# Kernel tuning notes

Measured on AMD Instinct MI355X. Metric: run time of the kernel, lower is better.

The kernel has to match this reference:

```python
import jax, jax.numpy as jnp
import numpy as np

B, C, H, W = 4, 256, 64, 64
R, KH, KW = 4, 3, 3
K = KH * KW  # 9 kernel taps


def _conv2d(x, w, b):
    # plain 3x3 conv, stride 1, pad 1, NCHW
    y = jax.lax.conv_general_dilated(x, w, (1, 1), ((1, 1), (1, 1)),
                                     dimension_numbers=('NCHW', 'OIHW', 'NCHW'))
    return y + b[None, :, None, None]


def _bilinear_sample(x, py, px):
    # x: [B,C,H,W]; py,px: [B,K,H,W] float coords; zero padding outside the image.
    B_, C_, H_, W_ = x.shape
    xf = x.reshape(B_, C_, H_ * W_)
    y0 = jnp.floor(py)
    x0 = jnp.floor(px)
    wy = py - y0
    wx = px - x0
    y0i = y0.astype(jnp.int32)
    x0i = x0.astype(jnp.int32)

    def corner(yi, xi, wgt):
        valid = (yi >= 0) & (yi < H_) & (xi >= 0) & (xi < W_)
        idx = (jnp.clip(yi, 0, H_ - 1) * W_ + jnp.clip(xi, 0, W_ - 1)).reshape(B_, -1)
        vals = jax.vmap(lambda xb, ib: jnp.take(xb, ib, axis=1))(xf, idx)  # [B,C,K*H*W]
        vals = vals.reshape(B_, C_, K, H_, W_)
        w_ = (wgt * valid).astype(x.dtype)[:, None]  # [B,1,K,H,W]
        return vals * w_

    out = corner(y0i, x0i, (1 - wy) * (1 - wx))
    out = out + corner(y0i, x0i + 1, (1 - wy) * wx)
    out = out + corner(y0i + 1, x0i, wy * (1 - wx))
    out = out + corner(y0i + 1, x0i + 1, wy * wx)
    return out  # [B,C,K,H,W]


def _deform_conv(x, offset, weight):
    # DCNv1: offset [B, 2K, H, W], interleaved (dy, dx) per kernel tap.
    B_, C_, H_, W_ = x.shape
    off = offset.reshape(B_, K, 2, H_, W_)
    ky, kx = jnp.meshgrid(jnp.arange(KH), jnp.arange(KW), indexing='ij')
    base_y = (ky.reshape(K) - (KH - 1) // 2).astype(x.dtype)
    base_x = (kx.reshape(K) - (KW - 1) // 2).astype(x.dtype)
    py = (jnp.arange(H_, dtype=x.dtype)[None, None, :, None]
          + base_y[None, :, None, None] + off[:, :, 0])
    px = (jnp.arange(W_, dtype=x.dtype)[None, None, None, :]
          + base_x[None, :, None, None] + off[:, :, 1])
    sampled = _bilinear_sample(x, py, px)  # [B,C,K,H,W]
    wr = weight.reshape(weight.shape[0], C_, K)
    return jnp.einsum('bckhw,ock->bohw', sampled, wr)


def setup_inputs() -> dict:
    key = jax.random.key(0)
    k1, k2, k3 = jax.random.split(key, 3)
    x = jax.random.normal(k1, (B, C, H, W), jnp.float32)
    off_w = jax.random.normal(k2, (R, 2 * K, C, KH, KW), jnp.float32) * 0.01
    off_b = jnp.zeros((R, 2 * K), jnp.float32)
    w = jax.random.normal(k3, (R, C, C, KH, KW), jnp.float32) * (1.0 / np.sqrt(C * K))
    return {"x": x, "off_w": off_w, "off_b": off_b, "w": w}


def reference(x, off_w, off_b, w):
    for r in range(R):  # fixed small layer count
        offset = _conv2d(x, off_w[r], off_b[r])
        x = jax.nn.relu(_deform_conv(x, offset, w[r]))
    return x
```

## Files before the change

kernel.cpp:

```cpp
#include <hip/hip_runtime.h>


#define HW 4096

typedef __attribute__((ext_vector_type(8))) __bf16 bf16x8;
typedef __attribute__((ext_vector_type(4))) float f32x4;
typedef __attribute__((ext_vector_type(8))) unsigned short u16x8;

__device__ inline unsigned int f2bf_bits(float f) {
  unsigned int u = __float_as_uint(f);
  return (u + 0x7fffu + ((u >> 16) & 1u)) >> 16;
}

__device__ inline void wg_barrier_lds() {
  asm volatile("s_waitcnt lgkmcnt(0)" ::: "memory");
  __builtin_amdgcn_s_barrier();
  __builtin_amdgcn_sched_barrier(0);
}

__global__ __launch_bounds__(256) void wpack_kernel(
    const float* __restrict__ w, unsigned short* __restrict__ wph) {
  const int f = blockIdx.x * 256 + threadIdx.x;
  const int j  = f & 7;
  const int l  = (f >> 3) & 63;
  const int nt = (f >> 9) & 15;
  const int q  = (f >> 13) % 72;
  const int r  = f / 589824;
  const int n  = nt * 16 + (l & 15);
  const int kk = q * 32 + ((l >> 4) << 3) + j;
  const int c  = kk & 255, k = kk >> 8;
  wph[f] = (unsigned short)f2bf_bits(w[((r * 256 + n) * 256 + c) * 9 + k]);
}

__global__ __launch_bounds__(256) void offwpack_kernel(
    const float* __restrict__ offw, unsigned short* __restrict__ owph) {
  const int f = blockIdx.x * 256 + threadIdx.x;
  const int j  = f & 7;
  const int l  = (f >> 3) & 63;
  const int nt = (f >> 9) & 1;
  const int q  = (f >> 10) % 72;
  const int r  = f / 73728;
  const int n  = nt * 16 + (l & 15);
  const int kk = q * 32 + ((l >> 4) << 3) + j;
  const int c  = kk & 255, k = kk >> 8;
  const float v = (n < 18) ? offw[((r * 18 + n) * 256 + c) * 9 + k] : 0.f;
  owph[f] = (unsigned short)f2bf_bits(v);
}

__global__ __launch_bounds__(256) void xpose_kernel(
    const float* __restrict__ x, unsigned short* __restrict__ xh) {
  const int p0 = blockIdx.x * 64;
  const int c0 = blockIdx.y * 64;
  const int b  = blockIdx.z;
  __shared__ float sT[64][65];
  const int t = threadIdx.x;
  const int pj = t & 63, ci0 = (t >> 6) * 16;
  const float* __restrict__ xb = x + ((size_t)(b * 256 + c0)) * HW + p0;
#pragma unroll
  for (int u = 0; u < 16; ++u)
    sT[ci0 + u][pj] = xb[(size_t)(ci0 + u) * HW + pj];
  __syncthreads();
  const int pr = t >> 2, cs = (t & 3) * 16;
  u16x8 va, vb;
#pragma unroll
  for (int u = 0; u < 8; ++u) va[u] = (unsigned short)f2bf_bits(sT[cs + u][pr]);
#pragma unroll
  for (int u = 0; u < 8; ++u) vb[u] = (unsigned short)f2bf_bits(sT[cs + 8 + u][pr]);
  const size_t o = ((size_t)b * HW + p0 + pr) * 256 + c0 + cs;
  *(u16x8*)(xh + o) = va;
  *(u16x8*)(xh + o + 8) = vb;
}

__global__ __launch_bounds__(1024, 4) void deform_mfma(
    const unsigned short* __restrict__ xh,
    const unsigned short* __restrict__ owh,
    const float* __restrict__ offb,
    const unsigned short* __restrict__ wph,
    unsigned short* __restrict__ yth,
    float* __restrict__ outf) {
  const int gid = blockIdx.x;
  const int b = (gid & 7) >> 1;
  const int h = ((gid >> 3) << 1) | (gid & 1);
  const int t = threadIdx.x, lane = t & 63, wv = t >> 6;
  const int frow = lane & 15, quad = lane >> 4;
  const int sm = t >> 4, cg = t & 15;

  __shared__ __align__(16) unsigned char smem[55808];
  float* s_cw = (float*)smem;
  int*   s_ci = (int*)(smem + 9216);
  unsigned char* sAb = smem + 18432;
  float* s_off = (float*)(smem + 51200);

  {
    const int kv = wv >> 3, ntO = (wv >> 2) & 1, mtO = wv & 3;
    const int mO = mtO * 16 + frow;
    f32x4 aoc = {0.f, 0.f, 0.f, 0.f};
    const u16x8 z8 = {};
    const size_t xb = (size_t)b * HW;
    const u16x8* __restrict__ owp = (const u16x8*)owh;

#define OHLOAD(k, p, A, Bv)                                                 \
  {                                                                         \
    const int ky = (k) / 3 - 1, kx = (k) % 3 - 1;                           \
    const int hy = h + ky;                                                  \
    const int hyc = hy < 0 ? 0 : (hy > 63 ? 63 : hy);                       \
    const int mx = mO + kx;                                                 \
    const bool v = ((unsigned)hy < 64u) && ((unsigned)mx < 64u);            \
    const int cpx = mx < 0 ? 0 : (mx > 63 ? 63 : mx);                       \
    const size_t abase = (xb + (size_t)(hyc * 64 + cpx)) * 256              \
                         + quad * 8 + kv * 128 + (p) * 64;                  \
    _Pragma("unroll") for (int j = 0; j < 2; ++j) {                         \
      A[j] = *(const u16x8*)(xh + abase + j * 32);                          \
      if (!v) A[j] = z8;                                                    \
    }                                                                       \
    _Pragma("unroll") for (int j = 0; j < 2; ++j)                           \
      Bv[j] = owp[(((k) * 8 + kv * 4 + (p) * 2 + j) * 2 + ntO) * 64 + lane];\
  }

#define OHMFMA(A, Bv)                                                       \
  _Pragma("unroll") for (int j = 0; j < 2; ++j)                             \
    aoc = __builtin_amdgcn_mfma_f32_16x16x32_bf16(                          \
        __builtin_bit_cast(bf16x8, A[j]), __builtin_bit_cast(bf16x8, Bv[j]),\
        aoc, 0, 0, 0);

    u16x8 A0[2], Bv0[2], A1[2], Bv1[2];
    OHLOAD(0, 0, A0, Bv0)
    OHLOAD(0, 1, A1, Bv1)
    OHMFMA(A0, Bv0) OHLOAD(1, 0, A0, Bv0)
    OHMFMA(A1, Bv1) OHLOAD(1, 1, A1, Bv1)
    OHMFMA(A0, Bv0) OHLOAD(2, 0, A0, Bv0)
    OHMFMA(A1, Bv1) OHLOAD(2, 1, A1, Bv1)
    OHMFMA(A0, Bv0) OHLOAD(3, 0, A0, Bv0)
    OHMFMA(A1, Bv1) OHLOAD(3, 1, A1, Bv1)
    OHMFMA(A0, Bv0) OHLOAD(4, 0, A0, Bv0)
    OHMFMA(A1, Bv1) OHLOAD(4, 1, A1, Bv1)
    OHMFMA(A0, Bv0) OHLOAD(5, 0, A0, Bv0)
    OHMFMA(A1, Bv1) OHLOAD(5, 1, A1, Bv1)
    OHMFMA(A0, Bv0) OHLOAD(6, 0, A0, Bv0)
    OHMFMA(A1, Bv1) OHLOAD(6, 1, A1, Bv1)
    OHMFMA(A0, Bv0) OHLOAD(7, 0, A0, Bv0)
    OHMFMA(A1, Bv1) OHLOAD(7, 1, A1, Bv1)
    OHMFMA(A0, Bv0) OHLOAD(8, 0, A0, Bv0)
    OHMFMA(A1, Bv1) OHLOAD(8, 1, A1, Bv1)
    OHMFMA(A0, Bv0)
    OHMFMA(A1, Bv1)
#undef OHLOAD
#undef OHMFMA

    f32x4* redp = (f32x4*)(smem + 18432);
    if (kv == 1) redp[(mtO * 2 + ntO) * 64 + lane] = aoc;
    __syncthreads();
    if (kv == 0) {
      const f32x4 o = redp[(mtO * 2 + ntO) * 64 + lane];
      aoc[0] += o[0]; aoc[1] += o[1]; aoc[2] += o[2]; aoc[3] += o[3];
      const int oc = ntO * 16 + frow;
      if (oc < 18) {
        const float bv = offb[oc];
        const int mb = mtO * 16 + quad * 4;
#pragma unroll
        for (int r = 0; r < 4; ++r) s_off[oc * 64 + mb + r] = aoc[r] + bv;
      }
    }
    __syncthreads();
  }

  if (t < 576) {
    const int k = t >> 6, m = t & 63;
    const int ky = k / 3 - 1, kx = k % 3 - 1;
    const float dy = s_off[(2 * k) * 64 + m];
    const float dx = s_off[(2 * k + 1) * 64 + m];
    const float py = (float)(h + ky) + dy;
    const float px = (float)(m + kx) + dx;
    const float y0f = floorf(py), x0f = floorf(px);
    const float wy = py - y0f, wx = px - x0f;
    const int y0 = (int)y0f, x0 = (int)x0f;
#pragma unroll
    for (int j = 0; j < 4; ++j) {
      const int yi = y0 + (j >> 1), xi = x0 + (j & 1);
      const bool v = (yi >= 0) && (yi < 64) && (xi >= 0) && (xi < 64);
      const float wgt = ((j >> 1) ? wy : 1.f - wy) * ((j & 1) ? wx : 1.f - wx);
      s_cw[(k * 4 + j) * 64 + m] = v ? wgt : 0.f;
      const int yc = yi < 0 ? 0 : (yi > 63 ? 63 : yi);
      const int xc = xi < 0 ? 0 : (xi > 63 ? 63 : xi);
      s_ci[(k * 4 + j) * 64 + m] = yc * 64 + xc;
    }
  }
  __syncthreads();

  f32x4 acc[2][4];
#pragma unroll
  for (int mt = 0; mt < 2; ++mt)
#pragma unroll
    for (int nt = 0; nt < 4; ++nt) acc[mt][nt] = (f32x4){0.f, 0.f, 0.f, 0.f};

  const char* __restrict__ xbc = (const char*)(xh + (size_t)b * HW * 256);
  const u16x8* __restrict__ wp = (const u16x8*)wph;
  const int kv  = wv >> 3;
  const int wmh = (wv >> 2) & 1;
  const int wng = wv & 3;
  const int bfo = wng * 4;

  const int gs = ((sm & 3) << 1) | ((sm >> 2) & 1);
  const int wbA = sm * 128 + ((((cg >> 2) ^ gs)) << 4) + (cg & 3) * 4;
  const int wbL = wbA ^ 64;
  const int gr = ((frow & 3) << 1) | ((frow >> 2) & 1);
  const int rb0 = (wmh * 32 + frow) * 128 + ((quad ^ gr) << 4) + kv * 8192;
  const int rb1 = rb0 + 2048;

  unsigned int G0[4], G1[4];
  u16x8 Bc[4], Bn[4];
  float cwrC[4], cwrN[4];
  int cibC[4], cibN[4];
#pragma unroll
  for (int j = 0; j < 4; ++j) {
    cwrC[j] = s_cw[j * 64 + sm];
    cibC[j] = s_ci[j * 64 + sm] * 512;
  }
#pragma unroll
  for (int j = 0; j < 4; ++j)
    G0[j] = *(const unsigned int*)(xbc + cibC[j] + cg * 4);
#pragma unroll
  for (int j = 0; j < 4; ++j)
    G1[j] = *(const unsigned int*)(xbc + cibC[j] + 64 + cg * 4);
#pragma unroll
  for (int i = 0; i < 4; ++i)
    Bc[i] = wp[(kv * 16 + bfo + i) * 64 + lane];

#define COMBINE_STORE(Gx, BB)                                               \
  {                                                                         \
    float s0 = cwrC[0] * __uint_as_float(Gx[0] << 16);                      \
    float s1 = cwrC[0] * __uint_as_float(Gx[0] & 0xffff0000u);              \
    s0 = fmaf(cwrC[1], __uint_as_float(Gx[1] << 16), s0);                   \
    s1 = fmaf(cwrC[1], __uint_as_float(Gx[1] & 0xffff0000u), s1);           \
    s0 = fmaf(cwrC[2], __uint_as_float(Gx[2] << 16), s0);                   \
    s1 = fmaf(cwrC[2], __uint_as_float(Gx[2] & 0xffff0000u), s1);           \
    s0 = fmaf(cwrC[3], __uint_as_float(Gx[3] << 16), s0);                   \
    s1 = fmaf(cwrC[3], __uint_as_float(Gx[3] & 0xffff0000u), s1);           \
    const __bf16 hb0 = (__bf16)s0, hb1 = (__bf16)s1;                        \
    const unsigned int hv =                                                 \
        (unsigned int)__builtin_bit_cast(unsigned short, hb0) |             \
        ((unsigned int)__builtin_bit_cast(unsigned short, hb1) << 16);      \
    const float d0 = s0 - __uint_as_float(hv << 16);                        \
    const float d1 = s1 - __uint_as_float(hv & 0xffff0000u);                \
    const __bf16 lb0 = (__bf16)d0, lb1 = (__bf16)d1;                        \
    const unsigned int lv =                                                 \
        (unsigned int)__builtin_bit_cast(unsigned short, lb0) |             \
        ((unsigned int)__builtin_bit_cast(unsigned short, lb1) << 16);      \
    *(unsigned int*)(sAb + (BB) + wbA) = hv;                                \
    *(unsigned int*)(sAb + (BB) + wbL) = lv;                                \
  }

#define MFMA_BODY(PBv)                                                      \
  {                                                                         \
    bf16x8 ah[2], al[2];                                                    \
    ah[0] = __builtin_bit_cast(bf16x8, *(const u16x8*)(sAb + (PBv) + rb0)); \
    al[0] = __builtin_bit_cast(bf16x8,                                      \
                               *(const u16x8*)(sAb + (PBv) + (rb0 ^ 64)));  \
    ah[1] = __builtin_bit_cast(bf16x8, *(const u16x8*)(sAb + (PBv) + rb1)); \
    al[1] = __builtin_bit_cast(bf16x8,                                      \
                               *(const u16x8*)(sAb + (PBv) + (rb1 ^ 64)));  \
    __builtin_amdgcn_s_setprio(1);                                          \
    _Pragma("unroll") for (int nt = 0; nt < 4; ++nt) {                      \
      const bf16x8 bv = __builtin_bit_cast(bf16x8, Bc[nt]);                 \
      _Pragma("unroll") for (int mt = 0; mt < 2; ++mt) {                    \
        acc[mt][nt] = __builtin_amdgcn_mfma_f32_16x16x32_bf16(              \
            ah[mt], bv, acc[mt][nt], 0, 0, 0);                              \
        acc[mt][nt] = __builtin_amdgcn_mfma_f32_16x16x32_bf16(              \
            al[mt], bv, acc[mt][nt], 0, 0, 0);                              \
      }                                                                     \
    }                                                                       \
    __builtin_amdgcn_s_setprio(0);                                          \
  }

  for (int k9 = 0; k9 < 9; ++k9) {
#pragma unroll
    for (int sp = 0; sp < 4; ++sp) {
      const int PB = (sp & 1) * 16384;
      COMBINE_STORE(G0, PB)
      COMBINE_STORE(G1, PB + 8192)
      wg_barrier_lds();
      const bool more = (k9 < 8) || (sp < 3);
      if (more) {
        if (sp == 3) {
#pragma unroll
          for (int j = 0; j < 4; ++j) {
            cwrN[j] = s_cw[((k9 + 1) * 4 + j) * 64 + sm];
            cibN[j] = s_ci[((k9 + 1) * 4 + j) * 64 + sm] * 512;
          }
#pragma unroll
          for (int j = 0; j < 4; ++j)
            G0[j] = *(const unsigned int*)(xbc + cibN[j] + cg * 4);
#pragma unroll
          for (int j = 0; j < 4; ++j)
            G1[j] = *(const unsigned int*)(xbc + cibN[j] + 64 + cg * 4);
        } else {
          const int c0b = ((2 * sp + 2) & 7) * 64 + cg * 4;
#pragma unroll
          for (int j = 0; j < 4; ++j)
            G0[j] = *(const unsigned int*)(xbc + cibC[j] + c0b);
#pragma unroll
          for (int j = 0; j < 4; ++j)
            G1[j] = *(const unsigned int*)(xbc + cibC[j] + c0b + 64);
        }
      }
      MFMA_BODY(PB)
      if (more) {
        const int cn = k9 * 8 + 2 * sp + kv + 2;
#pragma unroll
        for (int i = 0; i < 4; ++i)
          Bn[i] = wp[(cn * 16 + bfo + i) * 64 + lane];
#pragma unroll
        for (int i = 0; i < 4; ++i) Bc[i] = Bn[i];
      }
      if (sp == 3 && k9 < 8) {
#pragma unroll
        for (int j = 0; j < 4; ++j) { cwrC[j] = cwrN[j]; cibC[j] = cibN[j]; }
      }
    }
  }
#undef COMBINE_STORE
#undef MFMA_BODY

  __syncthreads();
  {
    float* redb = (float*)sAb;
    const int rbase = ((wv & 7) * 64 + lane) * 16;
#pragma unroll
    for (int ph = 0; ph < 2; ++ph) {
      if (kv == 1) {
#pragma unroll
        for (int mt = 0; mt < 2; ++mt)
#pragma unroll
          for (int q2 = 0; q2 < 2; ++q2)
            *(f32x4*)&redb[rbase + (mt * 2 + q2) * 4] = acc[mt][ph * 2 + q2];
      }
      __syncthreads();
      if (kv == 0) {
#pragma unroll
        for (int mt = 0; mt < 2; ++mt)
#pragma unroll
          for (int q2 = 0; q2 < 2; ++q2) {
            const f32x4 o = *(const f32x4*)&redb[rbase + (mt * 2 + q2) * 4];
            acc[mt][ph * 2 + q2][0] += o[0];
            acc[mt][ph * 2 + q2][1] += o[1];
            acc[mt][ph * 2 + q2][2] += o[2];
            acc[mt][ph * 2 + q2][3] += o[3];
          }
      }
      __syncthreads();
    }
  }

  if (outf) {
    if (kv == 0) {
#pragma unroll
      for (int mt = 0; mt < 2; ++mt)
#pragma unroll
        for (int nt = 0; nt < 4; ++nt) {
          const int n = wng * 64 + nt * 16 + frow;
          const int pos = h * 64 + wmh * 32 + mt * 16 + quad * 4;
          float4 vv;
          vv.x = fmaxf(acc[mt][nt][0], 0.f);
          vv.y = fmaxf(acc[mt][nt][1], 0.f);
          vv.z = fmaxf(acc[mt][nt][2], 0.f);
          vv.w = fmaxf(acc[mt][nt][3], 0.f);
          *(float4*)&outf[(size_t)(b * 256 + n) * HW + pos] = vv;
        }
    }
  } else {
    unsigned short* sW = (unsigned short*)(smem + (wv & 7) * 4608);
    if (kv == 0) {
#pragma unroll
      for (int mt = 0; mt < 2; ++mt)
#pragma unroll
        for (int nt = 0; nt < 4; ++nt)
#pragma unroll
          for (int r = 0; r < 4; ++r)
            sW[(mt * 16 + quad * 4 + r) * 72 + nt * 16 + frow] =
                (unsigned short)f2bf_bits(fmaxf(acc[mt][nt][r], 0.f));
    }
    __syncthreads();
    if (kv == 0) {
      const int rowl = lane & 31, colh = lane >> 5;
      const int pos = h * 64 + wmh * 32 + rowl;
      unsigned short* __restrict__ yp =
          yth + ((size_t)b * HW + pos) * 256 + wng * 64 + colh * 32;
#pragma unroll
      for (int g = 0; g < 4; ++g)
        *(u16x8*)(yp + g * 8) = *(const u16x8*)&sW[rowl * 72 + colh * 32 + g * 8];
    }
  }
}

extern "C" void kernel_launch(void* const* d_in, const int* in_sizes, int n_in,
                              void* d_out, int out_size, void* d_ws, size_t ws_size,
                              hipStream_t stream) {
  const float* x0   = (const float*)d_in[0];
  const float* offw = (const float*)d_in[1];
  const float* offb = (const float*)d_in[2];
  const float* w    = (const float*)d_in[3];
  float* out = (float*)d_out;
  float* ws  = (float*)d_ws;

  unsigned short* wph  = (unsigned short*)(ws + 294912);
  unsigned short* owph = wph + 2359296;
  unsigned short* xTA  = owph + 294912;
  unsigned short* xTB  = xTA + 4194304;

  wpack_kernel<<<9216, 256, 0, stream>>>(w, wph);
  offwpack_kernel<<<1152, 256, 0, stream>>>(offw, owph);
  xpose_kernel<<<dim3(64, 4, 4), 256, 0, stream>>>(x0, xTA);

  unsigned short* pin = xTA;
  unsigned short* pout = xTB;
  for (int r = 0; r < 4; ++r) {
    deform_mfma<<<256, 1024, 0, stream>>>(pin, owph + r * 73728,
                                          offb + r * 18,
                                          wph + (size_t)r * 589824,
                                          (r < 3) ? pout : nullptr,
                                          (r < 3) ? nullptr : out);
    unsigned short* tmp = pin; pin = pout; pout = tmp;
  }
}
```

Measured before the change: 345.6 us.

## Stage four channel chunks per barrier to halve LDS sync count

The main loop now combines and stores four 64-channel chunks (half a tap's channels) per LDS barrier instead of two, using a 64 KB double buffer. This halves the workgroup barriers per tap from four to two and doubles the MFMA work between syncs. In exchange it uses more LDS (about 88 KB) and more registers for the extra gather and weight fragments, which may reduce occupancy or add register pressure.

```diff
diff --git a/kernel.cpp b/kernel.cpp
--- a/kernel.cpp
+++ b/kernel.cpp
@@ -85,11 +85,11 @@
   const int frow = lane & 15, quad = lane >> 4;
   const int sm = t >> 4, cg = t & 15;
 
-  __shared__ __align__(16) unsigned char smem[55808];
+  __shared__ __align__(16) unsigned char smem[88576];
   float* s_cw = (float*)smem;
   int*   s_ci = (int*)(smem + 9216);
   unsigned char* sAb = smem + 18432;
-  float* s_off = (float*)(smem + 51200);
+  float* s_off = (float*)(smem + 83968);
 
   {
     const int kv = wv >> 3, ntO = (wv >> 2) & 1, mtO = wv & 3;
@@ -204,11 +204,12 @@
   const int wbA = sm * 128 + ((((cg >> 2) ^ gs)) << 4) + (cg & 3) * 4;
   const int wbL = wbA ^ 64;
   const int gr = ((frow & 3) << 1) | ((frow >> 2) & 1);
-  const int rb0 = (wmh * 32 + frow) * 128 + ((quad ^ gr) << 4) + kv * 8192;
-  const int rb1 = rb0 + 2048;
-
-  unsigned int G0[4], G1[4];
-  u16x8 Bc[4], Bn[4];
+  const int rbM = (wmh * 32 + frow) * 128 + ((quad ^ gr) << 4);
+  const int rcA = kv * 8192;
+  const int rcB = rcA + 16384;
+
+  unsigned int G0[4], G1[4], G2[4], G3[4];
+  u16x8 Bc[4], Bd[4];
   float cwrC[4], cwrN[4];
   int cibC[4], cibN[4];
 #pragma unroll
@@ -223,8 +224,17 @@
   for (int j = 0; j < 4; ++j)
     G1[j] = *(const unsigned int*)(xbc + cibC[j] + 64 + cg * 4);
 #pragma unroll
+  for (int j = 0; j < 4; ++j)
+    G2[j] = *(const unsigned int*)(xbc + cibC[j] + 128 + cg * 4);
+#pragma unroll
+  for (int j = 0; j < 4; ++j)
+    G3[j] = *(const unsigned int*)(xbc + cibC[j] + 192 + cg * 4);
+#pragma unroll
   for (int i = 0; i < 4; ++i)
     Bc[i] = wp[(kv * 16 + bfo + i) * 64 + lane];
+#pragma unroll
+  for (int i = 0; i < 4; ++i)
+    Bd[i] = wp[((2 + kv) * 16 + bfo + i) * 64 + lane];
 
 #define COMBINE_STORE(Gx, BB)                                               \
   {                                                                         \
@@ -250,76 +260,110 @@
     *(unsigned int*)(sAb + (BB) + wbL) = lv;                                \
   }
 
-#define MFMA_BODY(PBv)                                                      \
+#define MFMA_BODY4(HB)                                                      \
   {                                                                         \
-    bf16x8 ah[2], al[2];                                                    \
-    ah[0] = __builtin_bit_cast(bf16x8, *(const u16x8*)(sAb + (PBv) + rb0)); \
-    al[0] = __builtin_bit_cast(bf16x8,                                      \
-                               *(const u16x8*)(sAb + (PBv) + (rb0 ^ 64)));  \
-    ah[1] = __builtin_bit_cast(bf16x8, *(const u16x8*)(sAb + (PBv) + rb1)); \
-    al[1] = __builtin_bit_cast(bf16x8,                                      \
-                               *(const u16x8*)(sAb + (PBv) + (rb1 ^ 64)));  \
+    bf16x8 ah0[2], al0[2], ah1[2], al1[2];                                  \
+    ah0[0] = __builtin_bit_cast(                                            \
+        bf16x8, *(const u16x8*)(sAb + (HB) + rcA + rbM));                   \
+    al0[0] = __builtin_bit_cast(                                            \
+        bf16x8, *(const u16x8*)(sAb + (HB) + rcA + (rbM ^ 64)));            \
+    ah0[1] = __builtin_bit_cast(                                            \
+        bf16x8, *(const u16x8*)(sAb + (HB) + rcA + rbM + 2048));            \
+    al0[1] = __builtin_bit_cast(                                            \
+        bf16x8, *(const u16x8*)(sAb + (HB) + rcA + ((rbM + 2048) ^ 64)));   \
+    ah1[0] = __builtin_bit_cast(                                            \
+        bf16x8, *(const u16x8*)(sAb + (HB) + rcB + rbM));                   \
+    al1[0] = __builtin_bit_cast(                                            \
+        bf16x8, *(const u16x8*)(sAb + (HB) + rcB + (rbM ^ 64)));            \
+    ah1[1] = __builtin_bit_cast(                                            \
+        bf16x8, *(const u16x8*)(sAb + (HB) + rcB + rbM + 2048));            \
+    al1[1] = __builtin_bit_cast(                                            \
+        bf16x8, *(const u16x8*)(sAb + (HB) + rcB + ((rbM + 2048) ^ 64)));   \
     __builtin_amdgcn_s_setprio(1);                                          \
     _Pragma("unroll") for (int nt = 0; nt < 4; ++nt) {                      \
       const bf16x8 bv = __builtin_bit_cast(bf16x8, Bc[nt]);                 \
       _Pragma("unroll") for (int mt = 0; mt < 2; ++mt) {                    \
         acc[mt][nt] = __builtin_amdgcn_mfma_f32_16x16x32_bf16(              \
-            ah[mt], bv, acc[mt][nt], 0, 0, 0);                              \
+            ah0[mt], bv, acc[mt][nt], 0, 0, 0);                             \
         acc[mt][nt] = __builtin_amdgcn_mfma_f32_16x16x32_bf16(              \
-            al[mt], bv, acc[mt][nt], 0, 0, 0);                              \
+            al0[mt], bv, acc[mt][nt], 0, 0, 0);                             \
+      }                                                                     \
+    }                                                                       \
+    _Pragma("unroll") for (int nt = 0; nt < 4; ++nt) {                      \
+      const bf16x8 bv = __builtin_bit_cast(bf16x8, Bd[nt]);                 \
+      _Pragma("unroll") for (int mt = 0; mt < 2; ++mt) {                    \
+        acc[mt][nt] = __builtin_amdgcn_mfma_f32_16x16x32_bf16(              \
+            ah1[mt], bv, acc[mt][nt], 0, 0, 0);                             \
+        acc[mt][nt] = __builtin_amdgcn_mfma_f32_16x16x32_bf16(              \
+            al1[mt], bv, acc[mt][nt], 0, 0, 0);                             \
       }                                                                     \
     }                                                                       \
     __builtin_amdgcn_s_setprio(0);                                          \
   }
 
+#define BADV2(cb)                                                           \
+  {                                                                         \
+    _Pragma("unroll") for (int i = 0; i < 4; ++i)                           \
+      Bc[i] = wp[(((cb) + kv) * 16 + bfo + i) * 64 + lane];                 \
+    _Pragma("unroll") for (int i = 0; i < 4; ++i)                           \
+      Bd[i] = wp[(((cb) + 2 + kv) * 16 + bfo + i) * 64 + lane];             \
+  }
+
   for (int k9 = 0; k9 < 9; ++k9) {
-#pragma unroll
-    for (int sp = 0; sp < 4; ++sp) {
-      const int PB = (sp & 1) * 16384;
-      COMBINE_STORE(G0, PB)
-      COMBINE_STORE(G1, PB + 8192)
-      wg_barrier_lds();
-      const bool more = (k9 < 8) || (sp < 3);
-      if (more) {
-        if (sp == 3) {
-#pragma unroll
-          for (int j = 0; j < 4; ++j) {
-            cwrN[j] = s_cw[((k9 + 1) * 4 + j) * 64 + sm];
-            cibN[j] = s_ci[((k9 + 1) * 4 + j) * 64 + sm] * 512;
-          }
-#pragma unroll
-          for (int j = 0; j < 4; ++j)
-            G0[j] = *(const unsigned int*)(xbc + cibN[j] + cg * 4);
-#pragma unroll
-          for (int j = 0; j < 4; ++j)
-            G1[j] = *(const unsigned int*)(xbc + cibN[j] + 64 + cg * 4);
-        } else {
-          const int c0b = ((2 * sp + 2) & 7) * 64 + cg * 4;
-#pragma unroll
-          for (int j = 0; j < 4; ++j)
-            G0[j] = *(const unsigned int*)(xbc + cibC[j] + c0b);
-#pragma unroll
-          for (int j = 0; j < 4; ++j)
-            G1[j] = *(const unsigned int*)(xbc + cibC[j] + c0b + 64);
-        }
+    const bool tapN = (k9 < 8);
+    COMBINE_STORE(G0, 0)
+    COMBINE_STORE(G1, 8192)
+    COMBINE_STORE(G2, 16384)
+    COMBINE_STORE(G3, 24576)
+    wg_barrier_lds();
+#pragma unroll
+    for (int j = 0; j < 4; ++j)
+      G0[j] = *(const unsigned int*)(xbc + cibC[j] + 256 + cg * 4);
+#pragma unroll
+    for (int j = 0; j < 4; ++j)
+      G1[j] = *(const unsigned int*)(xbc + cibC[j] + 320 + cg * 4);
+#pragma unroll
+    for (int j = 0; j < 4; ++j)
+      G2[j] = *(const unsigned int*)(xbc + cibC[j] + 384 + cg * 4);
+#pragma unroll
+    for (int j = 0; j < 4; ++j)
+      G3[j] = *(const unsigned int*)(xbc + cibC[j] + 448 + cg * 4);
+    MFMA_BODY4(0)
+    BADV2(k9 * 8 + 4)
+    COMBINE_STORE(G0, 32768)
+    COMBINE_STORE(G1, 40960)
+    COMBINE_STORE(G2, 49152)
+    COMBINE_STORE(G3, 57344)
+    wg_barrier_lds();
+    if (tapN) {
+#pragma unroll
+      for (int j = 0; j < 4; ++j) {
+        cwrN[j] = s_cw[((k9 + 1) * 4 + j) * 64 + sm];
+        cibN[j] = s_ci[((k9 + 1) * 4 + j) * 64 + sm] * 512;
       }
-      MFMA_BODY(PB)
-      if (more) {
-        const int cn = k9 * 8 + 2 * sp + kv + 2;
-#pragma unroll
-        for (int i = 0; i < 4; ++i)
-          Bn[i] = wp[(cn * 16 + bfo + i) * 64 + lane];
-#pragma unroll
-        for (int i = 0; i < 4; ++i) Bc[i] = Bn[i];
-      }
-      if (sp == 3 && k9 < 8) {
-#pragma unroll
-        for (int j = 0; j < 4; ++j) { cwrC[j] = cwrN[j]; cibC[j] = cibN[j]; }
-      }
+#pragma unroll
+      for (int j = 0; j < 4; ++j)
+        G0[j] = *(const unsigned int*)(xbc + cibN[j] + cg * 4);
+#pragma unroll
+      for (int j = 0; j < 4; ++j)
+        G1[j] = *(const unsigned int*)(xbc + cibN[j] + 64 + cg * 4);
+#pragma unroll
+      for (int j = 0; j < 4; ++j)
+        G2[j] = *(const unsigned int*)(xbc + cibN[j] + 128 + cg * 4);
+#pragma unroll
+      for (int j = 0; j < 4; ++j)
+        G3[j] = *(const unsigned int*)(xbc + cibN[j] + 192 + cg * 4);
+    }
+    MFMA_BODY4(32768)
+    if (tapN) {
+      BADV2((k9 + 1) * 8)
+#pragma unroll
+      for (int j = 0; j < 4; ++j) { cwrC[j] = cwrN[j]; cibC[j] = cibN[j]; }
     }
   }
 #undef COMBINE_STORE
-#undef MFMA_BODY
+#undef MFMA_BODY4
+#undef BADV2
 
   __syncthreads();
   {
```

After: 483.6 us. 40.0% more time.
